# Kernel optimization log

Measured on AMD Instinct MI355X. Metric: run time of the kernel, lower is better.

## Reference

```python
import jax, jax.numpy as jnp
import numpy as np

HEADS = 16
DIM_HEAD = 64

def setup_inputs() -> dict:
    key = jax.random.key(0)
    ks = jax.random.split(key, 7)
    B, Nq, Dq = 4, 2048, 1024
    Nk, Dc = 1024, 768
    inner = HEADS * DIM_HEAD  # 1024
    sq = 1.0 / np.sqrt(Dq)
    sc = 1.0 / np.sqrt(Dc)
    si = 1.0 / np.sqrt(inner)
    return {
        "x": jax.random.normal(ks[0], (B, Nq, Dq), dtype=jnp.float32),
        "context": jax.random.normal(ks[1], (B, Nk, Dc), dtype=jnp.float32),
        "Wq": jax.random.normal(ks[2], (Dq, inner), dtype=jnp.float32) * sq,
        "Wk": jax.random.normal(ks[3], (Dc, inner), dtype=jnp.float32) * sc,
        "Wv": jax.random.normal(ks[4], (Dc, inner), dtype=jnp.float32) * sc,
        "Wo": jax.random.normal(ks[5], (inner, Dq), dtype=jnp.float32) * si,
        "bo": jax.random.normal(ks[6], (Dq,), dtype=jnp.float32) * 0.01,
    }

def reference(x, context, Wq, Wk, Wv, Wo, bo):
    B, Nq, _ = x.shape
    Nk = context.shape[1]
    h, dh = HEADS, DIM_HEAD
    # projections (no bias on q/k/v, matching nn.Linear(bias=False))
    q = (x @ Wq).reshape(B, Nq, h, dh)        # [B,Nq,h,dh]
    k = (context @ Wk).reshape(B, Nk, h, dh)  # [B,Nk,h,dh]
    v = (context @ Wv).reshape(B, Nk, h, dh)
    scale = 1.0 / jnp.sqrt(jnp.asarray(dh, dtype=x.dtype))
    # scores: [B,h,Nq,Nk]
    scores = jnp.einsum('bqhd,bkhd->bhqk', q, k) * scale
    attn = jax.nn.softmax(scores, axis=-1)
    out = jnp.einsum('bhqk,bkhd->bqhd', attn, v).reshape(B, Nq, h * dh)
    return out @ Wo + bo
```

## Files before the change

kernel.cpp:

```cpp
#include <hip/hip_runtime.h>

typedef __bf16 bf16;
typedef __bf16 bf16x2 __attribute__((ext_vector_type(2)));
typedef __bf16 bf16x4 __attribute__((ext_vector_type(4)));
typedef __bf16 bf16x8 __attribute__((ext_vector_type(8)));
typedef float f32x4 __attribute__((ext_vector_type(4)));

#define MFMA(a, b, c) __builtin_amdgcn_mfma_f32_16x16x32_bf16(a, b, c, 0, 0, 0)

#define GLD16(gptr, ldsptr)                                                        \
  __builtin_amdgcn_global_load_lds(                                                \
      (const __attribute__((address_space(1))) unsigned int*)(gptr),               \
      (__attribute__((address_space(3))) unsigned int*)(ldsptr), 16, 0, 0)

union I4B8 { int4 i; bf16x8 v; };
union FI { float f; int i; };
union HI { bf16x2 h; int i; };

__global__ __launch_bounds__(256) void prep_k(const float* __restrict__ x, bf16* __restrict__ xb,
                                              const float* __restrict__ ctx, bf16* __restrict__ ctxb,
                                              const float* __restrict__ Wq, bf16* __restrict__ WqT,
                                              const float* __restrict__ Wk, bf16* __restrict__ WkvT,
                                              const float* __restrict__ Wv,
                                              const float* __restrict__ Wo, bf16* __restrict__ WoT) {
  __shared__ float t[32][33];
  const int bid = blockIdx.x;
  if (bid < 5632) {
    const float* in; bf16* out; size_t i;
    if (bid < 4096) { in = x; out = xb; i = ((size_t)bid * 256 + threadIdx.x) * 8; }
    else { in = ctx; out = ctxb; i = ((size_t)(bid - 4096) * 256 + threadIdx.x) * 8; }
    const float4 a = *(const float4*)(in + i);
    const float4 b = *(const float4*)(in + i + 4);
    bf16x8 o;
    o[0] = (bf16)a.x; o[1] = (bf16)a.y; o[2] = (bf16)a.z; o[3] = (bf16)a.w;
    o[4] = (bf16)b.x; o[5] = (bf16)b.y; o[6] = (bf16)b.z; o[7] = (bf16)b.w;
    *(bf16x8*)(out + i) = o;
    return;
  }
  const int tt = bid - 5632;
  const int z = tt >> 10, rem = tt & 1023;
  const float* in; bf16* out; int R; float sc = 1.0f;
  if (z == 0)      { in = Wq; out = WqT;                R = 1024; sc = 0.18033688f; }
  else if (z == 1) { in = Wk; out = WkvT;               R = 768; }
  else if (z == 2) { in = Wv; out = WkvT + 1024 * 768;  R = 768; }
  else             { in = Wo; out = WoT;                R = 1024; }
  const int c0 = (rem & 31) * 32, r0 = (rem >> 5) * 32;
  if (r0 >= R) return;
  const int tx = threadIdx.x & 31, ty = threadIdx.x >> 5;
#pragma unroll
  for (int i = 0; i < 4; i++)
    t[ty + i * 8][tx] = in[(size_t)(r0 + ty + i * 8) * 1024 + c0 + tx];
  __syncthreads();
#pragma unroll
  for (int i = 0; i < 4; i++)
    out[(size_t)(c0 + ty + i * 8) * R + r0 + tx] = (bf16)(t[tx][ty + i * 8] * sc);
}

template <int MODE, int TN>
__device__ __forceinline__ void gemm_body(const bf16* __restrict__ A,
                                          const bf16* __restrict__ Bt,
                                          int K, int m0, int n0,
                                          void* __restrict__ C0,
                                          const float* __restrict__ bias,
                                          bf16* As, bf16* Bs) {
  constexpr int NI = TN / 32;
  const int tid = threadIdx.x;
  const int lane = tid & 63, wave = tid >> 6;
  const int wm = wave >> 1, wn = wave & 1;
  const int q = lane >> 4, c = lane & 15;

  f32x4 acc[4][NI] = {};
  const bf16* Ag = A + (size_t)(m0 + (tid >> 2)) * K + (tid & 3) * 8;
  const bf16* Bg = Bt + (size_t)(n0 + (tid >> 2)) * K + (tid & 3) * 8;
  const size_t K64 = (size_t)K * 64;
  bf16* AsW = &As[wave * 512];
  bf16* BsW = &Bs[wave * 512];

  for (int k0 = 0; k0 < K; k0 += 32) {
    __syncthreads();
    GLD16(Ag + k0, AsW);
    GLD16(Ag + k0 + K64, AsW + 2048);
    GLD16(Bg + k0, BsW);
    if constexpr (TN == 128) GLD16(Bg + k0 + K64, BsW + 2048);
    __syncthreads();
    bf16x8 af[4], bfr[NI];
#pragma unroll
    for (int mi = 0; mi < 4; mi++)
      af[mi] = *(const bf16x8*)&As[(wm * 64 + mi * 16 + c) * 32 + q * 8];
#pragma unroll
    for (int ni = 0; ni < NI; ni++)
      bfr[ni] = *(const bf16x8*)&Bs[(wn * (TN / 2) + ni * 16 + c) * 32 + q * 8];
#pragma unroll
    for (int mi = 0; mi < 4; mi++)
#pragma unroll
      for (int ni = 0; ni < NI; ni++) {
        if constexpr (MODE == 2)
          acc[mi][ni] = MFMA(af[mi], bfr[ni], acc[mi][ni]);
        else
          acc[mi][ni] = MFMA(bfr[ni], af[mi], acc[mi][ni]);
      }
  }

  if constexpr (MODE == 0 || MODE == 1) {
#pragma unroll
    for (int ni = 0; ni < NI; ni++) {
      const int col = n0 + wn * (TN / 2) + ni * 16 + q * 4;
      float4 bv4 = {};
      if constexpr (MODE == 1) bv4 = *(const float4*)&bias[col];
#pragma unroll
      for (int mi = 0; mi < 4; mi++) {
        const int row = m0 + wm * 64 + mi * 16 + c;
        if constexpr (MODE == 0) {
          bf16x4 vv;
#pragma unroll
          for (int r = 0; r < 4; r++) vv[r] = (bf16)acc[mi][ni][r];
          *(bf16x4*)&((bf16*)C0)[(size_t)row * 1024 + col] = vv;
        } else {
          f32x4 vv;
          vv[0] = acc[mi][ni][0] + bv4.x; vv[1] = acc[mi][ni][1] + bv4.y;
          vv[2] = acc[mi][ni][2] + bv4.z; vv[3] = acc[mi][ni][3] + bv4.w;
          *(f32x4*)&((float*)C0)[(size_t)row * 1024 + col] = vv;
        }
      }
    }
  } else {
#pragma unroll
    for (int ni = 0; ni < NI; ni++) {
      const int col = n0 + wn * (TN / 2) + ni * 16 + c;
#pragma unroll
      for (int mi = 0; mi < 4; mi++) {
        const int rbase = m0 + wm * 64 + mi * 16 + q * 4;
        const int b = rbase >> 10, key = rbase & 1023;
        bf16* VT = (bf16*)C0;
        const int h = col >> 6, d = col & 63;
        const int kl = key & 63;
        const int pkey = (key & ~63) | (kl & 32) | ((kl & 12) << 1) | ((kl & 16) >> 2);
        bf16x4 vv;
#pragma unroll
        for (int r = 0; r < 4; r++) vv[r] = (bf16)acc[mi][ni][r];
        *(bf16x4*)&VT[((size_t)(b * 16 + h) * 64 + d) * 1024 + pkey] = vv;
      }
    }
  }
}

__global__ __launch_bounds__(256) void proj_k(const bf16* __restrict__ xb,
                                              const bf16* __restrict__ ctxb,
                                              const bf16* __restrict__ WqT,
                                              const bf16* __restrict__ WkvT,
                                              bf16* __restrict__ Q,
                                              bf16* __restrict__ Kp,
                                              bf16* __restrict__ VT) {
  __shared__ __align__(16) bf16 As[4096];
  __shared__ __align__(16) bf16 Bs[4096];
  const int bid = blockIdx.x;
  if (bid < 512) {
    gemm_body<0, 128>(xb, WqT, 1024, (bid >> 3) * 128, (bid & 7) * 128, Q, nullptr, As, Bs);
  } else if (bid < 768) {
    const int b2 = bid - 512;
    gemm_body<0, 128>(ctxb, WkvT, 768, (b2 >> 3) * 128, (b2 & 7) * 128, Kp, nullptr, As, Bs);
  } else {
    const int b3 = bid - 768;
    gemm_body<2, 128>(ctxb, WkvT + (size_t)1024 * 768, 768, (b3 >> 3) * 128, (b3 & 7) * 128,
                      VT, nullptr, As, Bs);
  }
}

__global__ __launch_bounds__(256) void out_k(const bf16* __restrict__ O,
                                             const bf16* __restrict__ WoT,
                                             float* __restrict__ out,
                                             const float* __restrict__ bo) {
  __shared__ __align__(16) bf16 As[4096];
  __shared__ __align__(16) bf16 Bs[2048];
  const int bid = blockIdx.x;
  gemm_body<1, 64>(O, WoT, 1024, (bid >> 4) * 128, (bid & 15) * 64, out, bo, As, Bs);
}

__global__ __launch_bounds__(256) void attn_k(const bf16* __restrict__ Qg,
                                              const bf16* __restrict__ Kg,
                                              const bf16* __restrict__ VTg,
                                              bf16* __restrict__ Og) {
  __shared__ __align__(16) bf16 Ks[64][72];
  __shared__ __align__(16) bf16 Vt[64][72];
  const int tid = threadIdx.x;
  const int lane = tid & 63, w = tid >> 6;
  const int q = lane >> 4, c = lane & 15;
  const int head = blockIdx.y, b = blockIdx.z;
  const int q0 = blockIdx.x * 128;

  bf16x8 aQ[2][2];
#pragma unroll
  for (int mj = 0; mj < 2; mj++)
#pragma unroll
    for (int ks = 0; ks < 2; ks++)
      aQ[mj][ks] = *(const bf16x8*)(Qg + (size_t)(b * 2048 + q0 + w * 32 + mj * 16 + c) * 1024 +
                                    head * 64 + ks * 32 + q * 8);

  f32x4 o[2][4] = {};
  float lsum[2] = {0.f, 0.f};

  const int srow = tid >> 2, sc = tid & 3;
  const bf16* Kbase = Kg + (size_t)(b * 1024 + srow) * 1024 + head * 64 + sc * 16;
  const bf16* Vbase = VTg + ((size_t)(b * 16 + head) * 64 + srow) * 1024 + sc * 16;

  bf16x8 rk0 = *(const bf16x8*)(Kbase);
  bf16x8 rk1 = *(const bf16x8*)(Kbase + 8);
  bf16x8 rv0 = *(const bf16x8*)(Vbase);
  bf16x8 rv1 = *(const bf16x8*)(Vbase + 8);

  for (int kt = 0; kt < 16; kt++) {
    __syncthreads();
    *(bf16x8*)&Ks[srow][sc * 16]     = rk0;
    *(bf16x8*)&Ks[srow][sc * 16 + 8] = rk1;
    *(bf16x8*)&Vt[srow][sc * 16]     = rv0;
    *(bf16x8*)&Vt[srow][sc * 16 + 8] = rv1;
    if (kt < 15) {
      const size_t ko = (size_t)(kt + 1) * 64 * 1024;
      const int vo = (kt + 1) * 64;
      rk0 = *(const bf16x8*)(Kbase + ko);
      rk1 = *(const bf16x8*)(Kbase + ko + 8);
      rv0 = *(const bf16x8*)(Vbase + vo);
      rv1 = *(const bf16x8*)(Vbase + vo + 8);
    }
    __syncthreads();

    f32x4 st[2][4] = {};
#pragma unroll
    for (int ks = 0; ks < 2; ks++) {
      bf16x8 ak[4];
#pragma unroll
      for (int ni = 0; ni < 4; ni++) ak[ni] = *(const bf16x8*)&Ks[ni * 16 + c][ks * 32 + q * 8];
#pragma unroll
      for (int mj = 0; mj < 2; mj++)
#pragma unroll
        for (int ni = 0; ni < 4; ni++)
          st[mj][ni] = MFMA(ak[ni], aQ[mj][ks], st[mj][ni]);
    }

    int pk[2][4][2];
#pragma unroll
    for (int mj = 0; mj < 2; mj++)
#pragma unroll
      for (int ni = 0; ni < 4; ni++) {
        float p0 = __builtin_amdgcn_exp2f(st[mj][ni][0]);
        float p1 = __builtin_amdgcn_exp2f(st[mj][ni][1]);
        float p2 = __builtin_amdgcn_exp2f(st[mj][ni][2]);
        float p3 = __builtin_amdgcn_exp2f(st[mj][ni][3]);
        lsum[mj] += (p0 + p1) + (p2 + p3);
        HI h0, h1;
        h0.h[0] = (bf16)p0; h0.h[1] = (bf16)p1;
        h1.h[0] = (bf16)p2; h1.h[1] = (bf16)p3;
        pk[mj][ni][0] = h0.i;
        pk[mj][ni][1] = h1.i;
      }

#pragma unroll
    for (int ks2 = 0; ks2 < 2; ks2++) {
      bf16x8 bv[4];
#pragma unroll
      for (int ni = 0; ni < 4; ni++)
        bv[ni] = *(const bf16x8*)&Vt[ni * 16 + c][ks2 * 32 + q * 8];
#pragma unroll
      for (int mi = 0; mi < 2; mi++) {
        I4B8 pa;
        pa.i.x = pk[mi][2 * ks2][0];
        pa.i.y = pk[mi][2 * ks2][1];
        pa.i.z = pk[mi][2 * ks2 + 1][0];
        pa.i.w = pk[mi][2 * ks2 + 1][1];
#pragma unroll
        for (int ni = 0; ni < 4; ni++)
          o[mi][ni] = MFMA(pa.v, bv[ni], o[mi][ni]);
      }
    }
  }

  FI rl[2];
#pragma unroll
  for (int mj = 0; mj < 2; mj++) {
    float l = lsum[mj];
    l += __shfl_xor(l, 16, 64);
    l += __shfl_xor(l, 32, 64);
    rl[mj].f = 1.0f / l;
  }

#pragma unroll
  for (int mi = 0; mi < 2; mi++) {
    FI rli[4];
#pragma unroll
    for (int r = 0; r < 4; r++)
      rli[r].i = __builtin_amdgcn_ds_bpermute((q * 4 + r) << 2, rl[mi].i);
#pragma unroll
    for (int ni = 0; ni < 4; ni++)
#pragma unroll
      for (int r = 0; r < 4; r++) {
        const int qrow = q0 + w * 32 + mi * 16 + q * 4 + r;
        const int col = head * 64 + ni * 16 + c;
        Og[(size_t)(b * 2048 + qrow) * 1024 + col] = (bf16)(o[mi][ni][r] * rli[r].f);
      }
  }
}

extern "C" void kernel_launch(void* const* d_in, const int* in_sizes, int n_in,
                              void* d_out, int out_size, void* d_ws, size_t ws_size,
                              hipStream_t stream) {
  (void)in_sizes; (void)n_in; (void)out_size; (void)ws_size;
  const float* x   = (const float*)d_in[0];
  const float* ctx = (const float*)d_in[1];
  const float* Wq  = (const float*)d_in[2];
  const float* Wk  = (const float*)d_in[3];
  const float* Wv  = (const float*)d_in[4];
  const float* Wo  = (const float*)d_in[5];
  const float* bo  = (const float*)d_in[6];
  float* out = (float*)d_out;

  char* ws = (char*)d_ws;
  const size_t MB = 1u << 20;
  bf16* WqT  = (bf16*)(ws);
  bf16* WkvT = (bf16*)(ws + 2 * MB);
  bf16* WoT  = (bf16*)(ws + 5 * MB);
  bf16* ctxb = (bf16*)(ws + 7 * MB);
  bf16* xb   = (bf16*)(ws + 13 * MB);
  bf16* Q    = (bf16*)(ws + 29 * MB);
  bf16* Kp   = (bf16*)(ws + 45 * MB);
  bf16* VT   = (bf16*)(ws + 53 * MB);
  bf16* O    = xb;

  prep_k<<<5632 + 4096, 256, 0, stream>>>(x, xb, ctx, ctxb, Wq, WqT, Wk, WkvT, Wv, Wo, WoT);

  proj_k<<<1024, 256, 0, stream>>>(xb, ctxb, WqT, WkvT, Q, Kp, VT);

  attn_k<<<dim3(16, 16, 4), 256, 0, stream>>>(Q, Kp, VT, O);

  out_k<<<1024, 256, 0, stream>>>(O, WoT, out, bo);
}
```

Measured before the change: 236.0 us.

## Remap block order for XCD locality, widen out GEMM tile, MFMA row sums

```diff
diff --git a/kernel.cpp b/kernel.cpp
--- a/kernel.cpp
+++ b/kernel.cpp
@@ -14,7 +14,6 @@
       (__attribute__((address_space(3))) unsigned int*)(ldsptr), 16, 0, 0)
 
 union I4B8 { int4 i; bf16x8 v; };
-union FI { float f; int i; };
 union HI { bf16x2 h; int i; };
 
 __global__ __launch_bounds__(256) void prep_k(const float* __restrict__ x, bf16* __restrict__ xb,
@@ -155,13 +154,16 @@
   __shared__ __align__(16) bf16 Bs[4096];
   const int bid = blockIdx.x;
   if (bid < 512) {
-    gemm_body<0, 128>(xb, WqT, 1024, (bid >> 3) * 128, (bid & 7) * 128, Q, nullptr, As, Bs);
+    const int s = (bid & 7) * 64 + (bid >> 3);
+    gemm_body<0, 128>(xb, WqT, 1024, (s >> 3) * 128, (s & 7) * 128, Q, nullptr, As, Bs);
   } else if (bid < 768) {
-    const int b2 = bid - 512;
-    gemm_body<0, 128>(ctxb, WkvT, 768, (b2 >> 3) * 128, (b2 & 7) * 128, Kp, nullptr, As, Bs);
+    const int t = bid - 512;
+    const int s = (t & 7) * 32 + (t >> 3);
+    gemm_body<0, 128>(ctxb, WkvT, 768, (s >> 3) * 128, (s & 7) * 128, Kp, nullptr, As, Bs);
   } else {
-    const int b3 = bid - 768;
-    gemm_body<2, 128>(ctxb, WkvT + (size_t)1024 * 768, 768, (b3 >> 3) * 128, (b3 & 7) * 128,
+    const int t = bid - 768;
+    const int s = (t & 7) * 32 + (t >> 3);
+    gemm_body<2, 128>(ctxb, WkvT + (size_t)1024 * 768, 768, (s >> 3) * 128, (s & 7) * 128,
                       VT, nullptr, As, Bs);
   }
 }
@@ -171,9 +173,10 @@
                                              float* __restrict__ out,
                                              const float* __restrict__ bo) {
   __shared__ __align__(16) bf16 As[4096];
-  __shared__ __align__(16) bf16 Bs[2048];
+  __shared__ __align__(16) bf16 Bs[4096];
   const int bid = blockIdx.x;
-  gemm_body<1, 64>(O, WoT, 1024, (bid >> 4) * 128, (bid & 15) * 64, out, bo, As, Bs);
+  const int s = (bid & 7) * 64 + (bid >> 3);
+  gemm_body<1, 128>(O, WoT, 1024, (s >> 3) * 128, (s & 7) * 128, out, bo, As, Bs);
 }
 
 __global__ __launch_bounds__(256) void attn_k(const bf16* __restrict__ Qg,
@@ -185,8 +188,10 @@
   const int tid = threadIdx.x;
   const int lane = tid & 63, w = tid >> 6;
   const int q = lane >> 4, c = lane & 15;
-  const int head = blockIdx.y, b = blockIdx.z;
-  const int q0 = blockIdx.x * 128;
+  const int bid = blockIdx.x;
+  const int pair = (bid & 7) * 8 + (bid >> 7);
+  const int head = pair & 15, b = pair >> 4;
+  const int q0 = ((bid >> 3) & 15) * 128;
 
   bf16x8 aQ[2][2];
 #pragma unroll
@@ -197,7 +202,10 @@
                                     head * 64 + ks * 32 + q * 8);
 
   f32x4 o[2][4] = {};
-  float lsum[2] = {0.f, 0.f};
+  f32x4 ol[2] = {};
+  bf16x8 vone;
+#pragma unroll
+  for (int i = 0; i < 8; i++) vone[i] = (bf16)1.0f;
 
   const int srow = tid >> 2, sc = tid & 3;
   const bf16* Kbase = Kg + (size_t)(b * 1024 + srow) * 1024 + head * 64 + sc * 16;
@@ -230,11 +238,13 @@
       bf16x8 ak[4];
 #pragma unroll
       for (int ni = 0; ni < 4; ni++) ak[ni] = *(const bf16x8*)&Ks[ni * 16 + c][ks * 32 + q * 8];
+      __builtin_amdgcn_s_setprio(1);
 #pragma unroll
       for (int mj = 0; mj < 2; mj++)
 #pragma unroll
         for (int ni = 0; ni < 4; ni++)
           st[mj][ni] = MFMA(ak[ni], aQ[mj][ks], st[mj][ni]);
+      __builtin_amdgcn_s_setprio(0);
     }
 
     int pk[2][4][2];
@@ -246,7 +256,6 @@
         float p1 = __builtin_amdgcn_exp2f(st[mj][ni][1]);
         float p2 = __builtin_amdgcn_exp2f(st[mj][ni][2]);
         float p3 = __builtin_amdgcn_exp2f(st[mj][ni][3]);
-        lsum[mj] += (p0 + p1) + (p2 + p3);
         HI h0, h1;
         h0.h[0] = (bf16)p0; h0.h[1] = (bf16)p1;
         h1.h[0] = (bf16)p2; h1.h[1] = (bf16)p3;
@@ -267,35 +276,28 @@
         pa.i.y = pk[mi][2 * ks2][1];
         pa.i.z = pk[mi][2 * ks2 + 1][0];
         pa.i.w = pk[mi][2 * ks2 + 1][1];
+        __builtin_amdgcn_s_setprio(1);
 #pragma unroll
         for (int ni = 0; ni < 4; ni++)
           o[mi][ni] = MFMA(pa.v, bv[ni], o[mi][ni]);
-      }
-    }
-  }
-
-  FI rl[2];
-#pragma unroll
-  for (int mj = 0; mj < 2; mj++) {
-    float l = lsum[mj];
-    l += __shfl_xor(l, 16, 64);
-    l += __shfl_xor(l, 32, 64);
-    rl[mj].f = 1.0f / l;
+        ol[mi] = MFMA(pa.v, vone, ol[mi]);
+        __builtin_amdgcn_s_setprio(0);
+      }
+    }
   }
 
 #pragma unroll
   for (int mi = 0; mi < 2; mi++) {
-    FI rli[4];
-#pragma unroll
-    for (int r = 0; r < 4; r++)
-      rli[r].i = __builtin_amdgcn_ds_bpermute((q * 4 + r) << 2, rl[mi].i);
+    float inv[4];
+#pragma unroll
+    for (int r = 0; r < 4; r++) inv[r] = 1.0f / ol[mi][r];
 #pragma unroll
     for (int ni = 0; ni < 4; ni++)
 #pragma unroll
       for (int r = 0; r < 4; r++) {
         const int qrow = q0 + w * 32 + mi * 16 + q * 4 + r;
         const int col = head * 64 + ni * 16 + c;
-        Og[(size_t)(b * 2048 + qrow) * 1024 + col] = (bf16)(o[mi][ni][r] * rli[r].f);
+        Og[(size_t)(b * 2048 + qrow) * 1024 + col] = (bf16)(o[mi][ni][r] * inv[r]);
       }
   }
 }
@@ -329,7 +331,7 @@
 
   proj_k<<<1024, 256, 0, stream>>>(xb, ctxb, WqT, WkvT, Q, Kp, VT);
 
-  attn_k<<<dim3(16, 16, 4), 256, 0, stream>>>(Q, Kp, VT, O);
-
-  out_k<<<1024, 256, 0, stream>>>(O, WoT, out, bo);
-}
+  attn_k<<<1024, 256, 0, stream>>>(Q, Kp, VT, O);
+
+  out_k<<<512, 256, 0, stream>>>(O, WoT, out, bo);
+}
```

Measured after the change: 223.8 us. 1.05x faster.
